# Kernel optimization log

Measured on AMD Instinct MI355X. Metric: run time of the kernel, lower is better.

## Reference

```python
import jax, jax.numpy as jnp
import numpy as np

N, E, F_IN, H, C = 50000, 800000, 128, 4, 32
NEG_SLOPE = 0.2
BN_EPS = 1e-5


def setup_inputs() -> dict:
    key = jax.random.key(0)
    ks = jax.random.split(key, 6)
    x = jax.random.normal(ks[0], (N, F_IN), dtype=jnp.float32)
    edge_index = jax.random.randint(ks[1], (2, E), 0, N, dtype=jnp.int64)
    W = jax.random.normal(ks[2], (H * C, F_IN), dtype=jnp.float32) * (1.0 / np.sqrt(F_IN))
    att_src = jax.random.normal(ks[3], (H, C), dtype=jnp.float32) * 0.1
    att_dst = jax.random.normal(ks[4], (H, C), dtype=jnp.float32) * 0.1
    bias = jnp.zeros((H * C,), dtype=jnp.float32)
    gamma = jnp.ones((H * C,), dtype=jnp.float32)
    beta = jnp.zeros((H * C,), dtype=jnp.float32)
    return {"x": x, "edge_index": edge_index, "W": W, "att_src": att_src,
            "att_dst": att_dst, "bias": bias, "gamma": gamma, "beta": beta}


def reference(x, edge_index, W, att_src, att_dst, bias, gamma, beta):
    n = x.shape[0]
    loop = jnp.arange(n, dtype=edge_index.dtype)
    src = jnp.concatenate([edge_index[0], loop])  # add_self_loops=True (PyG default)
    dst = jnp.concatenate([edge_index[1], loop])
    # Linear projection (lin has no bias in GATConv)
    h = (x @ W.T).reshape(n, H, C)                      # [N,H,C]
    a_src = jnp.einsum('nhc,hc->nh', h, att_src)        # [N,H]
    a_dst = jnp.einsum('nhc,hc->nh', h, att_dst)
    e = jax.nn.leaky_relu(a_src[src] + a_dst[dst], NEG_SLOPE)  # [E+N,H]
    # segment softmax over incoming edges of each dst node
    emax = jax.ops.segment_max(e, dst, num_segments=n)
    emax = jnp.where(jnp.isfinite(emax), emax, 0.0)
    ex = jnp.exp(e - emax[dst])
    denom = jax.ops.segment_sum(ex, dst, num_segments=n)
    alpha = ex / (denom[dst] + 1e-16)                   # [E+N,H]
    msg = h[src] * alpha[:, :, None]                    # [E+N,H,C]
    out = jax.ops.segment_sum(msg, dst, num_segments=n).reshape(n, H * C) + bias
    out = jax.nn.relu(out)
    # BatchNorm1d over node dimension (training-mode batch stats)
    mean = out.mean(axis=0)
    var = out.var(axis=0)
    out = (out - mean) * jax.lax.rsqrt(var + BN_EPS) * gamma + beta
    return out
```

## Files before the change

### kernel.cpp

```cpp
#include <hip/hip_runtime.h>
#include <hip/hip_bf16.h>

#define HEADS 4
#define FDIM 128
#define NEG_SLOPE 0.2f
#define BN_EPS 1e-5f
#define CAP 3072
#define NB 512
#define NSLOT 32

typedef __attribute__((ext_vector_type(8))) short s8v;
typedef __attribute__((ext_vector_type(4))) float f4v;

__device__ __forceinline__ float lrelu(float x) { return x >= 0.f ? x : NEG_SLOPE * x; }

__device__ __forceinline__ unsigned short f2bf(float f) {
    unsigned int u = __float_as_uint(f);
    unsigned int r = (u + 0x7fffu + ((u >> 16) & 1u)) >> 16;
    return (unsigned short)r;
}
__device__ __forceinline__ float bflo(unsigned int u) { return __uint_as_float(u << 16); }
__device__ __forceinline__ float bfhi(unsigned int u) { return __uint_as_float(u & 0xffff0000u); }

__global__ __launch_bounds__(256) void k1_gemm_count(
    const float* __restrict__ x, const float* __restrict__ W,
    const float* __restrict__ att_src, const float* __restrict__ att_dst,
    const int* __restrict__ ei,
    unsigned short* __restrict__ hb, float* __restrict__ a_src,
    float* __restrict__ a_dst, int* __restrict__ cnts,
    int n, int E, int nbuk, int cpb, int gb)
{
    __shared__ uint4 bsh[2048];
    __shared__ int shi[512];
    int t = threadIdx.x;

    if ((int)blockIdx.x >= gb) {
        int cbid = blockIdx.x - gb;
        for (int i = t; i < nbuk; i += 256) shi[i] = 0;
        __syncthreads();
        int e0 = cbid * cpb, e1 = min(E, e0 + cpb);
        for (int e = e0 + t; e < e1; e += 256) atomicAdd(&shi[ei[E + e] >> 7], 1);
        __syncthreads();
        for (int i = t; i < nbuk; i += 256) cnts[cbid * nbuk + i] = shi[i];
        return;
    }

    for (int i = t; i < 2048; i += 256) {
        int l = i & 63, kt = (i >> 6) & 3, nt = i >> 8;
        int nrow = nt * 16 + (l & 15);
        int kb = kt * 32 + ((l >> 4) << 3);
        const float* src = W + nrow * FDIM + kb;
        float4 f0 = *(const float4*)src, f1 = *(const float4*)(src + 4);
        unsigned u0 = f2bf(f0.x) | ((unsigned)f2bf(f0.y) << 16);
        unsigned u1 = f2bf(f0.z) | ((unsigned)f2bf(f0.w) << 16);
        unsigned u2 = f2bf(f1.x) | ((unsigned)f2bf(f1.y) << 16);
        unsigned u3 = f2bf(f1.z) | ((unsigned)f2bf(f1.w) << 16);
        bsh[i] = make_uint4(u0, u1, u2, u3);
    }
    __syncthreads();

    int l = t & 63, wid = t >> 6;
    int r_base = blockIdx.x * 64 + wid * 16;
    int rg = l >> 4, l15 = l & 15;
    int row_in = r_base + l15;
    int rd = row_in < n ? row_in : 0;

    f4v acc[8];
#pragma unroll
    for (int i = 0; i < 8; ++i) acc[i] = (f4v){0.f, 0.f, 0.f, 0.f};
#pragma unroll
    for (int kt = 0; kt < 4; ++kt) {
        const float4* xp = (const float4*)(x + (size_t)rd * FDIM + kt * 32 + (rg << 3));
        float4 f0 = xp[0], f1 = xp[1];
        s8v a;
        a[0] = (short)f2bf(f0.x); a[1] = (short)f2bf(f0.y);
        a[2] = (short)f2bf(f0.z); a[3] = (short)f2bf(f0.w);
        a[4] = (short)f2bf(f1.x); a[5] = (short)f2bf(f1.y);
        a[6] = (short)f2bf(f1.z); a[7] = (short)f2bf(f1.w);
#pragma unroll
        for (int nt = 0; nt < 8; ++nt) {
            s8v b = *(const s8v*)&bsh[(nt * 4 + kt) * 64 + l];
            acc[nt] = __builtin_amdgcn_mfma_f32_16x16x32_bf16(a, b, acc[nt], 0, 0, 0);
        }
    }

    float asv[8], adv[8];
#pragma unroll
    for (int nt = 0; nt < 8; ++nt) {
        asv[nt] = att_src[nt * 16 + l15];
        adv[nt] = att_dst[nt * 16 + l15];
    }
#pragma unroll
    for (int r = 0; r < 4; ++r) {
        int row = r_base + rg * 4 + r;
        float ps[HEADS], pd[HEADS];
#pragma unroll
        for (int h = 0; h < HEADS; ++h) {
            ps[h] = acc[2 * h][r] * asv[2 * h] + acc[2 * h + 1][r] * asv[2 * h + 1];
            pd[h] = acc[2 * h][r] * adv[2 * h] + acc[2 * h + 1][r] * adv[2 * h + 1];
        }
#pragma unroll
        for (int d = 1; d < 16; d <<= 1) {
#pragma unroll
            for (int h = 0; h < HEADS; ++h) {
                ps[h] += __shfl_xor(ps[h], d);
                pd[h] += __shfl_xor(pd[h], d);
            }
        }
        if (l15 == 0 && row < n) {
            *(float4*)&a_src[row * HEADS] = make_float4(ps[0], ps[1], ps[2], ps[3]);
            *(float4*)&a_dst[row * HEADS] = make_float4(pd[0], pd[1], pd[2], pd[3]);
        }
    }
#pragma unroll
    for (int nt = 0; nt < 8; ++nt) {
#pragma unroll
        for (int r = 0; r < 4; ++r) {
            int row = r_base + rg * 4 + r;
            if (row < n) hb[(size_t)row * FDIM + nt * 16 + l15] = f2bf(acc[nt][r]);
        }
    }
}

__global__ __launch_bounds__(256) void k2_scanblk(const int* __restrict__ cnts,
                                                  int* __restrict__ bases,
                                                  int* __restrict__ sizes, int nbuk) {
    __shared__ int tmp[512];
    int b = blockIdx.x, t = threadIdx.x;
    int v0 = cnts[t * nbuk + b];
    int v1 = cnts[(t + 256) * nbuk + b];
    tmp[t] = v0; tmp[t + 256] = v1;
    __syncthreads();
    for (int s = 1; s < 512; s <<= 1) {
        int x0 = (t >= s) ? tmp[t - s] : 0;
        int x1 = (t + 256 >= s) ? tmp[t + 256 - s] : 0;
        __syncthreads();
        tmp[t] += x0; tmp[t + 256] += x1;
        __syncthreads();
    }
    bases[t * nbuk + b] = tmp[t] - v0;
    bases[(t + 256) * nbuk + b] = tmp[t + 256] - v1;
    if (t == 255) sizes[b] = tmp[511];
}

__global__ __launch_bounds__(1024) void k3_bucket_scan(
    const int* __restrict__ ei, const int* __restrict__ bases,
    const int* __restrict__ sizes, unsigned int* __restrict__ bucketed,
    int* __restrict__ goffs, int* __restrict__ offs,
    float* __restrict__ slotbuf,
    int N, int E, int nbuk, int cpb)
{
    __shared__ int lb[512];
    __shared__ int lr[512];
    int t = threadIdx.x;
    if ((int)blockIdx.x == NB) {
        int v = 0;
        if (t < 512) { v = (t < nbuk) ? sizes[t] : 0; lb[t] = v; }
        __syncthreads();
        for (int s = 1; s < 512; s <<= 1) {
            int x = (t < 512 && t >= s) ? lb[t - s] : 0;
            __syncthreads();
            if (t < 512) lb[t] += x;
            __syncthreads();
        }
        if (t < nbuk) goffs[t] = lb[t] - v;
        if (t == 0) { goffs[nbuk] = E; offs[N] = E; }
        for (int i = t; i < NSLOT * 256; i += 1024) slotbuf[i] = 0.f;
        return;
    }
    int bid = blockIdx.x;
    for (int i = t; i < nbuk; i += 1024) { lb[i] = bases[bid * nbuk + i]; lr[i] = 0; }
    __syncthreads();
    int e0 = bid * cpb, e1 = min(E, e0 + cpb);
    for (int e = e0 + t; e < e1; e += 1024) {
        int s = ei[e], d = ei[E + e];
        int b = d >> 7;
        int r = atomicAdd(&lr[b], 1);
        int p = lb[b] + r;
        if (p < CAP)
            bucketed[(size_t)b * CAP + p] = ((unsigned)(d & 127) << 16) | (unsigned)s;
    }
}

__global__ __launch_bounds__(256) void k4_csr(const unsigned int* __restrict__ bucketed,
                                              const int* __restrict__ sizes,
                                              const int* __restrict__ goffs,
                                              int* __restrict__ offs,
                                              unsigned short* __restrict__ csr, int N) {
    __shared__ int cnt[512], loff[512], tmp[512];
    int b = blockIdx.x, t = threadIdx.x;
    int sz = min(sizes[b], CAP), gbase = goffs[b];
    cnt[t] = 0; cnt[t + 256] = 0;
    __syncthreads();
    const unsigned int* seg = bucketed + (size_t)b * CAP;
    for (int j = t; j < sz; j += 256) {
        unsigned rec = seg[j];
        int key = (int)((rec >> 16) << 2) | (int)((rec & 0xffffu) >> 14);
        atomicAdd(&cnt[key], 1);
    }
    __syncthreads();
    tmp[t] = cnt[t]; tmp[t + 256] = cnt[t + 256];
    __syncthreads();
    for (int s = 1; s < 512; s <<= 1) {
        int x0 = (t >= s) ? tmp[t - s] : 0;
        int x1 = (t + 256 >= s) ? tmp[t + 256 - s] : 0;
        __syncthreads();
        tmp[t] += x0; tmp[t + 256] += x1;
        __syncthreads();
    }
    loff[t] = tmp[t] - cnt[t];
    loff[t + 256] = tmp[t + 256] - cnt[t + 256];
    if (t < 128) {
        int node = b * 128 + t;
        if (node < N) offs[node] = gbase + tmp[4 * t] - cnt[4 * t];
    }
    __syncthreads();
    for (int j = t; j < sz; j += 256) {
        unsigned rec = seg[j];
        int src = (int)(rec & 0xffffu);
        int key = (int)((rec >> 16) << 2) | (src >> 14);
        int pos = atomicAdd(&loff[key], 1);
        csr[gbase + pos] = (unsigned short)src;
    }
}

#define AGG_E(S, EW)                                                         \
    {                                                                        \
        uint4 u_ = *(const uint4*)&hb[(size_t)(S) * FDIM + c8];              \
        acc0.x += (EW) * bflo(u_.x); acc0.y += (EW) * bfhi(u_.x);            \
        acc0.z += (EW) * bflo(u_.y); acc0.w += (EW) * bfhi(u_.y);            \
        acc1.x += (EW) * bflo(u_.z); acc1.y += (EW) * bfhi(u_.z);            \
        acc1.z += (EW) * bflo(u_.w); acc1.w += (EW) * bfhi(u_.w);            \
        denom += (EW);                                                       \
    }

#define ACC2(E0, U0, E1, U1)                                                 \
    acc0.x += (E0) * bflo((U0).x) + (E1) * bflo((U1).x);                     \
    acc0.y += (E0) * bfhi((U0).x) + (E1) * bfhi((U1).x);                     \
    acc0.z += (E0) * bflo((U0).y) + (E1) * bflo((U1).y);                     \
    acc0.w += (E0) * bfhi((U0).y) + (E1) * bfhi((U1).y);                     \
    acc1.x += (E0) * bflo((U0).z) + (E1) * bflo((U1).z);                     \
    acc1.y += (E0) * bfhi((U0).z) + (E1) * bfhi((U1).z);                     \
    acc1.z += (E0) * bflo((U0).w) + (E1) * bflo((U1).w);                     \
    acc1.w += (E0) * bfhi((U0).w) + (E1) * bfhi((U1).w);

__global__ __launch_bounds__(256) void k5_agg(
    const unsigned short* __restrict__ hb, const float* __restrict__ a_src,
    const float* __restrict__ a_dst, const int* __restrict__ offs,
    const unsigned short* __restrict__ csr, const float* __restrict__ bias,
    unsigned short* __restrict__ outb, int n)
{
    int lane = threadIdx.x & 63;
    int node = blockIdx.x * 4 + (threadIdx.x >> 6);
    if (node >= n) return;
    int g = lane >> 4;
    int q = lane & 15;
    int c8 = q * 8;
    int head = q >> 2;

    float ad = a_dst[node * HEADS + head];
    int beg = offs[node], end = offs[node + 1];

    float4 acc0 = make_float4(0.f, 0.f, 0.f, 0.f);
    float4 acc1 = make_float4(0.f, 0.f, 0.f, 0.f);
    float denom = 0.f;

    if (g == 0) {
        float e_ = __expf(lrelu(a_src[node * HEADS + head] + ad));
        AGG_E(node, e_);
    }

    int j = beg + g;
    for (; j + 12 < end; j += 16) {
        int s0 = csr[j], s1 = csr[j + 4], s2 = csr[j + 8], s3 = csr[j + 12];
        float A0 = a_src[s0 * HEADS + head];
        float A1 = a_src[s1 * HEADS + head];
        float A2 = a_src[s2 * HEADS + head];
        float A3 = a_src[s3 * HEADS + head];
        uint4 u0 = *(const uint4*)&hb[(size_t)s0 * FDIM + c8];
        uint4 u1 = *(const uint4*)&hb[(size_t)s1 * FDIM + c8];
        uint4 u2 = *(const uint4*)&hb[(size_t)s2 * FDIM + c8];
        uint4 u3 = *(const uint4*)&hb[(size_t)s3 * FDIM + c8];
        float e0 = __expf(lrelu(A0 + ad));
        float e1 = __expf(lrelu(A1 + ad));
        float e2 = __expf(lrelu(A2 + ad));
        float e3 = __expf(lrelu(A3 + ad));
        ACC2(e0, u0, e1, u1);
        ACC2(e2, u2, e3, u3);
        denom += e0 + e1 + e2 + e3;
    }
    for (; j + 4 < end; j += 8) {
        int s0 = csr[j], s1 = csr[j + 4];
        float A0 = a_src[s0 * HEADS + head];
        float A1 = a_src[s1 * HEADS + head];
        uint4 u0 = *(const uint4*)&hb[(size_t)s0 * FDIM + c8];
        uint4 u1 = *(const uint4*)&hb[(size_t)s1 * FDIM + c8];
        float e0 = __expf(lrelu(A0 + ad));
        float e1 = __expf(lrelu(A1 + ad));
        ACC2(e0, u0, e1, u1);
        denom += e0 + e1;
    }
    for (; j < end; j += 4) {
        int s0 = csr[j];
        float e0 = __expf(lrelu(a_src[s0 * HEADS + head] + ad));
        AGG_E(s0, e0);
    }

#pragma unroll
    for (int d = 16; d < 64; d <<= 1) {
        acc0.x += __shfl_xor(acc0.x, d);
        acc0.y += __shfl_xor(acc0.y, d);
        acc0.z += __shfl_xor(acc0.z, d);
        acc0.w += __shfl_xor(acc0.w, d);
        acc1.x += __shfl_xor(acc1.x, d);
        acc1.y += __shfl_xor(acc1.y, d);
        acc1.z += __shfl_xor(acc1.z, d);
        acc1.w += __shfl_xor(acc1.w, d);
        denom += __shfl_xor(denom, d);
    }

    if (g == 0) {
        float inv = 1.f / (denom + 1e-16f);
        float4 b0 = *(const float4*)&bias[c8];
        float4 b1 = *(const float4*)&bias[c8 + 4];
        float o0 = fmaxf(acc0.x * inv + b0.x, 0.f);
        float o1 = fmaxf(acc0.y * inv + b0.y, 0.f);
        float o2 = fmaxf(acc0.z * inv + b0.z, 0.f);
        float o3 = fmaxf(acc0.w * inv + b0.w, 0.f);
        float o4 = fmaxf(acc1.x * inv + b1.x, 0.f);
        float o5 = fmaxf(acc1.y * inv + b1.y, 0.f);
        float o6 = fmaxf(acc1.z * inv + b1.z, 0.f);
        float o7 = fmaxf(acc1.w * inv + b1.w, 0.f);
        uint4 p;
        p.x = (unsigned)f2bf(o0) | ((unsigned)f2bf(o1) << 16);
        p.y = (unsigned)f2bf(o2) | ((unsigned)f2bf(o3) << 16);
        p.z = (unsigned)f2bf(o4) | ((unsigned)f2bf(o5) << 16);
        p.w = (unsigned)f2bf(o6) | ((unsigned)f2bf(o7) << 16);
        ((uint4*)outb)[(size_t)node * 16 + q] = p;
    }
}

__global__ __launch_bounds__(256) void bn_sums(const unsigned short* __restrict__ outb,
                                               float* __restrict__ slotbuf, int n) {
    int t = threadIdx.x;
    int q = t & 31, rh = t >> 5;
    float4 s = make_float4(0.f, 0.f, 0.f, 0.f);
    float4 s2 = make_float4(0.f, 0.f, 0.f, 0.f);
    const uint2* o2 = (const uint2*)outb;
    for (int r = blockIdx.x * 8 + rh; r < n; r += gridDim.x * 8) {
        uint2 u = o2[(size_t)r * 32 + q];
        float4 v = make_float4(bflo(u.x), bfhi(u.x), bflo(u.y), bfhi(u.y));
        s.x += v.x; s.y += v.y; s.z += v.z; s.w += v.w;
        s2.x += v.x * v.x; s2.y += v.y * v.y; s2.z += v.z * v.z; s2.w += v.w * v.w;
    }
    __shared__ float4 sh[2][8][32];
    sh[0][rh][q] = s;
    sh[1][rh][q] = s2;
    __syncthreads();
    if (rh == 0) {
#pragma unroll
        for (int i = 1; i < 8; ++i) {
            float4 a = sh[0][i][q], b = sh[1][i][q];
            s.x += a.x; s.y += a.y; s.z += a.z; s.w += a.w;
            s2.x += b.x; s2.y += b.y; s2.z += b.z; s2.w += b.w;
        }
        float* slot = slotbuf + (blockIdx.x & (NSLOT - 1)) * 256;
        atomicAdd(&slot[q * 4 + 0], s.x);
        atomicAdd(&slot[q * 4 + 1], s.y);
        atomicAdd(&slot[q * 4 + 2], s.z);
        atomicAdd(&slot[q * 4 + 3], s.w);
        atomicAdd(&slot[128 + q * 4 + 0], s2.x);
        atomicAdd(&slot[128 + q * 4 + 1], s2.y);
        atomicAdd(&slot[128 + q * 4 + 2], s2.z);
        atomicAdd(&slot[128 + q * 4 + 3], s2.w);
    }
}

__global__ __launch_bounds__(256) void k6_bn_apply(
    float* __restrict__ out, const unsigned short* __restrict__ outb,
    const float* __restrict__ slotbuf,
    const float* __restrict__ gamma, const float* __restrict__ beta, int N)
{
    __shared__ __align__(16) float sc[FDIM], sh[FDIM];
    int t = threadIdx.x;
    if (t < FDIM) {
        float s = 0.f, s2 = 0.f;
#pragma unroll
        for (int k = 0; k < NSLOT; ++k) {
            s  += slotbuf[k * 256 + t];
            s2 += slotbuf[k * 256 + 128 + t];
        }
        float mean = s / (float)N;
        float var = fmaxf(s2 / (float)N - mean * mean, 0.f);
        float g = gamma[t] * rsqrtf(var + BN_EPS);
        sc[t] = g;
        sh[t] = beta[t] - mean * g;
    }
    __syncthreads();
    int n4 = N * 32;
    const uint2* o2 = (const uint2*)outb;
    for (int i = blockIdx.x * 256 + t; i < n4; i += gridDim.x * 256) {
        uint2 u = o2[i];
        float4 v = make_float4(bflo(u.x), bfhi(u.x), bflo(u.y), bfhi(u.y));
        int f = (i & 31) * 4;
        float4 s4 = *(const float4*)&sc[f];
        float4 h4 = *(const float4*)&sh[f];
        v.x = v.x * s4.x + h4.x;
        v.y = v.y * s4.y + h4.y;
        v.z = v.z * s4.z + h4.z;
        v.w = v.w * s4.w + h4.w;
        ((float4*)out)[i] = v;
    }
}

static inline size_t align256(size_t x) { return (x + 255) & ~(size_t)255; }

extern "C" void kernel_launch(void* const* d_in, const int* in_sizes, int n_in,
                              void* d_out, int out_size, void* d_ws, size_t ws_size,
                              hipStream_t stream) {
    const float* x       = (const float*)d_in[0];
    const int*   ei      = (const int*)d_in[1];
    const float* W       = (const float*)d_in[2];
    const float* att_src = (const float*)d_in[3];
    const float* att_dst = (const float*)d_in[4];
    const float* bias    = (const float*)d_in[5];
    const float* gamma   = (const float*)d_in[6];
    const float* beta    = (const float*)d_in[7];
    float* out = (float*)d_out;

    int N = in_sizes[0] / FDIM;
    int E = in_sizes[1] / 2;
    int nbuk = (N + 127) >> 7;
    int cpb = (E + NB - 1) / NB;
    int gb = (N + 63) / 64;

    char* w = (char*)d_ws;
    unsigned short* hb = (unsigned short*)w;  w += align256((size_t)N * FDIM * 2);
    float* a_src  = (float*)w;  w += align256((size_t)N * HEADS * 4);
    float* a_dst  = (float*)w;  w += align256((size_t)N * HEADS * 4);
    int*   offs   = (int*)w;    w += align256((size_t)(N + 1) * 4);
    int*   cnts   = (int*)w;    w += align256((size_t)NB * nbuk * 4);
    int*   bases  = (int*)w;    w += align256((size_t)NB * nbuk * 4);
    int*   sizes  = (int*)w;    w += align256((size_t)nbuk * 4);
    int*   goffs  = (int*)w;    w += align256((size_t)(nbuk + 1) * 4);
    unsigned int* bucketed = (unsigned int*)w;  w += align256((size_t)nbuk * CAP * 4);
    unsigned short* csr = (unsigned short*)w;   w += align256((size_t)E * 2);
    unsigned short* outb = (unsigned short*)w;  w += align256((size_t)N * FDIM * 2);
    float* slotbuf = (float*)w; w += align256((size_t)NSLOT * 256 * 4);

    k1_gemm_count<<<gb + NB, 256, 0, stream>>>(x, W, att_src, att_dst, ei,
                                               hb, a_src, a_dst, cnts,
                                               N, E, nbuk, cpb, gb);
    k2_scanblk<<<nbuk, 256, 0, stream>>>(cnts, bases, sizes, nbuk);
    k3_bucket_scan<<<NB + 1, 1024, 0, stream>>>(ei, bases, sizes, bucketed,
                                                goffs, offs, slotbuf,
                                                N, E, nbuk, cpb);
    k4_csr<<<nbuk, 256, 0, stream>>>(bucketed, sizes, goffs, offs, csr, N);
    k5_agg<<<(N + 3) / 4, 256, 0, stream>>>(hb, a_src, a_dst, offs, csr, bias, outb, N);
    bn_sums<<<512, 256, 0, stream>>>(outb, slotbuf, N);
    k6_bn_apply<<<2048, 256, 0, stream>>>(out, outb, slotbuf, gamma, beta, N);
}
```

Before: 97.96 us.

## Locally sort edges per block before bucket scatter; simplify CSR node keys

The bucket-scatter kernel now counts destination buckets in shared memory, prefix-scans them, and stages records in shared memory grouped by bucket. It then writes each bucket's records contiguously, replacing scattered per-edge global writes with mostly coalesced ones. The CSR build kernel drops the secondary sort by source high bits and keys only on the 128 local destination nodes, which shrinks the scan. In exchange, neighbor lists are no longer grouped by source range, which may reduce cache locality in the aggregation gather. The shared record buffer also assumes each block handles at most 2048 edges.

```diff
diff --git a/kernel.cpp b/kernel.cpp
--- a/kernel.cpp
+++ b/kernel.cpp
@@ -151,7 +151,10 @@
     int N, int E, int nbuk, int cpb)
 {
     __shared__ int lb[512];
-    __shared__ int lr[512];
+    __shared__ int cnt[512];
+    __shared__ int bscan[512];
+    __shared__ int loff[512];
+    __shared__ unsigned recs[2048];
     int t = threadIdx.x;
     if ((int)blockIdx.x == NB) {
         int v = 0;
@@ -169,16 +172,45 @@
         return;
     }
     int bid = blockIdx.x;
-    for (int i = t; i < nbuk; i += 1024) { lb[i] = bases[bid * nbuk + i]; lr[i] = 0; }
+    if (t < 512) {
+        lb[t] = (t < nbuk) ? bases[bid * nbuk + t] : 0;
+        cnt[t] = 0;
+    }
     __syncthreads();
     int e0 = bid * cpb, e1 = min(E, e0 + cpb);
+    int szblk = e1 - e0;
+    unsigned myrec[2]; int myb[2]; int nmine = 0;
     for (int e = e0 + t; e < e1; e += 1024) {
         int s = ei[e], d = ei[E + e];
         int b = d >> 7;
-        int r = atomicAdd(&lr[b], 1);
-        int p = lb[b] + r;
+        myrec[nmine] = ((unsigned)b << 23) | ((unsigned)(d & 127) << 16) | (unsigned)s;
+        myb[nmine] = b;
+        ++nmine;
+        atomicAdd(&cnt[b], 1);
+    }
+    __syncthreads();
+    if (t < 512) bscan[t] = cnt[t];
+    __syncthreads();
+    for (int s = 1; s < 512; s <<= 1) {
+        int x = (t < 512 && t >= s) ? bscan[t - s] : 0;
+        __syncthreads();
+        if (t < 512) bscan[t] += x;
+        __syncthreads();
+    }
+    if (t < 512) loff[t] = bscan[t] - cnt[t];
+    __syncthreads();
+    for (int k = 0; k < nmine; ++k) {
+        int pos = atomicAdd(&loff[myb[k]], 1);
+        recs[pos] = myrec[k];
+    }
+    __syncthreads();
+    for (int i = t; i < szblk; i += 1024) {
+        unsigned rec = recs[i];
+        int b = rec >> 23;
+        int local = i - (bscan[b] - cnt[b]);
+        int p = lb[b] + local;
         if (p < CAP)
-            bucketed[(size_t)b * CAP + p] = ((unsigned)(d & 127) << 16) | (unsigned)s;
+            bucketed[(size_t)b * CAP + p] = rec & 0x7fffffu;
     }
 }
 
@@ -187,40 +219,33 @@
                                               const int* __restrict__ goffs,
                                               int* __restrict__ offs,
                                               unsigned short* __restrict__ csr, int N) {
-    __shared__ int cnt[512], loff[512], tmp[512];
+    __shared__ int cnt[128], loff[128], tmp[128];
     int b = blockIdx.x, t = threadIdx.x;
     int sz = min(sizes[b], CAP), gbase = goffs[b];
-    cnt[t] = 0; cnt[t + 256] = 0;
+    if (t < 128) cnt[t] = 0;
     __syncthreads();
     const unsigned int* seg = bucketed + (size_t)b * CAP;
+    for (int j = t; j < sz; j += 256) atomicAdd(&cnt[(seg[j] >> 16) & 127], 1);
+    __syncthreads();
+    if (t < 128) tmp[t] = cnt[t];
+    __syncthreads();
+    for (int s = 1; s < 128; s <<= 1) {
+        int x = (t < 128 && t >= s) ? tmp[t - s] : 0;
+        __syncthreads();
+        if (t < 128) tmp[t] += x;
+        __syncthreads();
+    }
+    if (t < 128) {
+        loff[t] = tmp[t] - cnt[t];
+        int node = b * 128 + t;
+        if (node < N) offs[node] = gbase + loff[t];
+    }
+    __syncthreads();
     for (int j = t; j < sz; j += 256) {
         unsigned rec = seg[j];
-        int key = (int)((rec >> 16) << 2) | (int)((rec & 0xffffu) >> 14);
-        atomicAdd(&cnt[key], 1);
-    }
-    __syncthreads();
-    tmp[t] = cnt[t]; tmp[t + 256] = cnt[t + 256];
-    __syncthreads();
-    for (int s = 1; s < 512; s <<= 1) {
-        int x0 = (t >= s) ? tmp[t - s] : 0;
-        int x1 = (t + 256 >= s) ? tmp[t + 256 - s] : 0;
-        __syncthreads();
-        tmp[t] += x0; tmp[t + 256] += x1;
-        __syncthreads();
-    }
-    loff[t] = tmp[t] - cnt[t];
-    loff[t + 256] = tmp[t + 256] - cnt[t + 256];
-    if (t < 128) {
-        int node = b * 128 + t;
-        if (node < N) offs[node] = gbase + tmp[4 * t] - cnt[4 * t];
-    }
-    __syncthreads();
-    for (int j = t; j < sz; j += 256) {
-        unsigned rec = seg[j];
-        int src = (int)(rec & 0xffffu);
-        int key = (int)((rec >> 16) << 2) | (src >> 14);
-        int pos = atomicAdd(&loff[key], 1);
-        csr[gbase + pos] = (unsigned short)src;
+        int nd = (rec >> 16) & 127;
+        int pos = atomicAdd(&loff[nd], 1);
+        csr[gbase + pos] = (unsigned short)(rec & 0xffffu);
     }
 }
 
```

New measurement: 98.07 us. No clear change (+0.1%).
